# Performance work log

Hardware: AMD Instinct MI355X
Metric: run time of the kernel (lower is better)

## Reference

```python
import jax, jax.numpy as jnp
import numpy as np
from jax import lax

B, F, N = 1024, 512, 8  # batch, feature_dim, num_of_subAttention


def setup_inputs() -> dict:
    key = jax.random.key(0)
    ks = jax.random.split(key, 8)
    sc = 0.02
    return {
        "vx": jax.random.normal(ks[0], (B, F), dtype=jnp.float32),
        "ax": jax.random.normal(ks[1], (B, F), dtype=jnp.float32),
        # stacked per-unit MLP params (N units)
        "W1": jax.random.normal(ks[2], (N, F, 2 * F), dtype=jnp.float32) * sc,
        "b1": jnp.zeros((N, F), jnp.float32),
        "W2": jax.random.normal(ks[3], (N, F, F), dtype=jnp.float32) * sc,
        "b2": jnp.zeros((N, F), jnp.float32),
        # conv pipeline params (OIHW)
        "conv1_w": jax.random.normal(ks[4], (F, F, 3, 3), dtype=jnp.float32) * sc,
        "conv1_b": jnp.zeros((F,), jnp.float32),
        "conv2_w": jax.random.normal(ks[5], (F, F, 3, 3), dtype=jnp.float32) * sc,
        "conv2_b": jnp.zeros((F,), jnp.float32),
    }


def reference(vx, ax, W1, b1, W2, b2, conv1_w, conv1_b, conv2_w, conv2_b):
    # --- N AttentionUnits, vectorized over the unit axis n ---
    x = jnp.concatenate([vx, ax], axis=-1)                      # [B, 2F]
    # Dropout(0.5) is identity in eval mode.
    h = jax.nn.relu(jnp.einsum('bi,nfi->bnf', x, W1) + b1)      # [B, N, F]
    att = jax.nn.relu(jnp.einsum('bnf,ngf->bng', h, W2) + b2)   # [B, N, F]

    # vx broadcast over units, elementwise attention, then permute to [B, F, N]
    va = jnp.transpose(vx[:, None, :] * att, (0, 2, 1))         # [B, F, N]
    # rank-1 broadcast along trailing axis -> conv input [B, F, N, N]
    t = jnp.broadcast_to(va[..., None], (B, F, N, N))

    dn = ('NCHW', 'OIHW', 'NCHW')
    y = lax.conv_general_dilated(t, conv1_w, (1, 1), 'SAME', dimension_numbers=dn)
    y = y + conv1_b[None, :, None, None]
    k = N // 2
    y = lax.reduce_window(y, -jnp.inf, lax.max, (1, 1, k, k), (1, 1, k, k), 'VALID')  # [B,F,2,2]
    y = lax.conv_general_dilated(y, conv2_w, (1, 1), 'SAME', dimension_numbers=dn)
    y = y + conv2_b[None, :, None, None]
    y = jnp.mean(y, axis=(2, 3))                                # AdaptiveAvgPool2d((1,1)) -> [B, F]
    return jax.nn.relu(y)
```

## Files before the change

### kernel.cpp

```cpp
#include <hip/hip_runtime.h>
#include <hip/hip_bf16.h>


typedef __attribute__((ext_vector_type(8))) short short8;
typedef __attribute__((ext_vector_type(4))) float f32x4;

__device__ __forceinline__ void gload16(const void* g, void* l) {
    __builtin_amdgcn_global_load_lds(
        (const __attribute__((address_space(1))) void*)g,
        (__attribute__((address_space(3))) void*)l, 16, 0, 0);
}

template<int BM, int BN, bool RELU, bool BIAS, bool OUT_BF16>
__global__ __launch_bounds__(256) void gemm_mfma(
    const __hip_bfloat16* __restrict__ A, int lda, long sA,
    const __hip_bfloat16* __restrict__ B, int ldb, long sB,
    void* __restrict__ Cv, int ldc, long sC,
    const float* __restrict__ bias, long sBias,
    int K)
{
    constexpr int MI = BM / 32, NI = BN / 32;
    constexpr int GA = BM / 16, GB = BN / 16;
    constexpr int nA = (GA * 2) / 4, nB = (GB * 2) / 4;
    __shared__ __align__(16) char As[128 * BM];
    __shared__ __align__(16) char Bs[128 * BN];

    const int z = blockIdx.z;
    A += (long)z * sA;
    B += (long)z * sB;
    const int bm = blockIdx.y * BM;
    const int bn = blockIdx.x * BN;
    const int t = threadIdx.x, lane = t & 63, wid = t >> 6;
    const int q = lane >> 4, lr = lane & 15;
    const int wrow = (wid >> 1) * (BM / 2), wcol = (wid & 1) * (BN / 2);

    const int m_loc = lane >> 2;
    const int cst = ((lane & 3) - (m_loc >> 1)) & 3;
    const long abase = ((long)(bm + m_loc) * lda + cst * 8) * 2;
    const long bbase = ((long)(bn + m_loc) * ldb + cst * 8) * 2;
    const int ro = lr * 4;
    const int csel = (lr >> 1);

    f32x4 acc[MI][NI] = {};

    for (int k0 = 0; k0 < K; k0 += 64) {
        if (k0) __syncthreads();
        #pragma unroll
        for (int i = 0; i < nA; ++i) {
            int s = wid * nA + i, g = s % GA, h = s / GA;
            gload16((const char*)A + abase + ((long)g * 16 * lda + h * 32 + k0) * 2,
                    As + (h * (BM * 4) + g * 64) * 16);
        }
        #pragma unroll
        for (int i = 0; i < nB; ++i) {
            int s = wid * nB + i, g = s % GB, h = s / GB;
            gload16((const char*)B + bbase + ((long)g * 16 * ldb + h * 32 + k0) * 2,
                    Bs + (h * (BN * 4) + g * 64) * 16);
        }
        __syncthreads();

        #pragma unroll
        for (int ks = 0; ks < 2; ++ks) {
            short8 af[MI], bf[NI];
            #pragma unroll
            for (int mi = 0; mi < MI; ++mi) {
                int u = ks * (BM * 4) + ((wrow >> 4) + mi) * 64 + ro + ((q + csel) & 3);
                af[mi] = *(const short8*)(As + u * 16);
            }
            #pragma unroll
            for (int ni = 0; ni < NI; ++ni) {
                int u = ks * (BN * 4) + ((wcol >> 4) + ni) * 64 + ro + ((q + csel) & 3);
                bf[ni] = *(const short8*)(Bs + u * 16);
            }
            #pragma unroll
            for (int mi = 0; mi < MI; ++mi)
                #pragma unroll
                for (int ni = 0; ni < NI; ++ni)
                    acc[mi][ni] = __builtin_amdgcn_mfma_f32_16x16x32_bf16(
                        af[mi], bf[ni], acc[mi][ni], 0, 0, 0);
        }
    }

    #pragma unroll
    for (int mi = 0; mi < MI; ++mi) {
        #pragma unroll
        for (int ni = 0; ni < NI; ++ni) {
            int gn = bn + wcol + ni * 16 + lr;
            float bv = 0.f;
            if constexpr (BIAS) bv = bias[z * sBias + gn];
            #pragma unroll
            for (int r = 0; r < 4; ++r) {
                long gm = bm + wrow + mi * 16 + q * 4 + r;
                float v = acc[mi][ni][r] + bv;
                if constexpr (RELU) v = fmaxf(v, 0.f);
                if constexpr (OUT_BF16)
                    ((__hip_bfloat16*)Cv)[z * sC + gm * ldc + gn] = __float2bfloat16(v);
                else
                    ((float*)Cv)[z * sC + gm * ldc + gn] = v;
            }
        }
    }
}

__global__ __launch_bounds__(256) void conv_gemm_pool(
    const float* __restrict__ vx,
    const __hip_bfloat16* __restrict__ att,
    const __hip_bfloat16* __restrict__ B,
    float* __restrict__ PM)
{
    constexpr int BM = 128, BN = 128, MI = 4, NI = 4;
    constexpr int GB = 8, nB = 4;
    const int ldb = 1536;
    __shared__ __align__(16) char VAs[160 * 144];
    __shared__ __align__(16) char Bs[128 * BN];

    const int bm = blockIdx.x * BM;
    const int bn = blockIdx.y * BN;
    const int t = threadIdx.x, lane = t & 63, wid = t >> 6;
    const int q = lane >> 4, lr = lane & 15;
    const int wrow = (wid >> 1) * 64, wcol = (wid & 1) * 64;

    const int m_loc = lane >> 2;
    const int cstB = ((lane & 3) - (m_loc >> 1)) & 3;
    const long bbase = ((long)(bn + m_loc) * ldb + cstB * 8) * 2;
    const int ro = lr * 4;
    const int csel = (lr >> 1);

    {
        int b = t >> 4, side = (t >> 3) & 1, w8 = t & 7;
        int pr = b * 10 + side * 9;
        short8 z8 = {0, 0, 0, 0, 0, 0, 0, 0};
        *(short8*)(VAs + (pr * 9 + w8) * 16) = z8;
    }

    int abase_[MI];
    #pragma unroll
    for (int mi = 0; mi < MI; ++mi) {
        int m = wrow + mi * 16 + lr;
        abase_[mi] = (((m >> 3) * 10 + (m & 7)) * 9 + q) * 16;
    }

    f32x4 acc[MI][NI] = {};

    for (int kk = 0; kk < 24; ++kk) {
        const int ki = kk - (kk / 3) * 3;
        const int c0 = (kk / 3) << 6;
        const int k0B = ki * 512 + c0;
        if (kk) __syncthreads();
        #pragma unroll
        for (int i = 0; i < nB; ++i) {
            int s = wid * nB + i, g = s % GB, h = s / GB;
            gload16((const char*)B + bbase + ((long)g * 16 * ldb + k0B + h * 32) * 2,
                    Bs + (h * (BN * 4) + g * 64) * 16);
        }
        if (ki == 0) {
            #pragma unroll
            for (int u = 0; u < 4; ++u) {
                int li = t + u * 256;
                int r = li >> 3, w8 = li & 7;
                int gm = bm + r;
                int c = c0 + w8 * 8;
                short8 a8 = *(const short8*)(att + (long)gm * 512 + c);
                const float* vp = vx + ((gm >> 3) << 9) + c;
                float4 v0 = *(const float4*)vp;
                float4 v1 = *(const float4*)(vp + 4);
                float vf[8] = {v0.x, v0.y, v0.z, v0.w, v1.x, v1.y, v1.z, v1.w};
                short8 val;
                #pragma unroll
                for (int j = 0; j < 8; ++j) {
                    union { short s; __hip_bfloat16 h; } ua; ua.s = a8[j];
                    union { __hip_bfloat16 h; short s; } ub;
                    ub.h = __float2bfloat16(__bfloat162float(ua.h) * vf[j]);
                    val[j] = ub.s;
                }
                int pr = (r >> 3) * 10 + 1 + (r & 7);
                *(short8*)(VAs + (pr * 9 + w8) * 16) = val;
            }
        }
        __syncthreads();

        #pragma unroll
        for (int ks = 0; ks < 2; ++ks) {
            short8 af[MI], bf[NI];
            #pragma unroll
            for (int mi = 0; mi < MI; ++mi)
                af[mi] = *(const short8*)(VAs + abase_[mi] + ki * 144 + ks * 64);
            #pragma unroll
            for (int ni = 0; ni < NI; ++ni) {
                int u = ks * (BN * 4) + ((wcol >> 4) + ni) * 64 + ro + ((q + csel) & 3);
                bf[ni] = *(const short8*)(Bs + u * 16);
            }
            #pragma unroll
            for (int mi = 0; mi < MI; ++mi)
                #pragma unroll
                for (int ni = 0; ni < NI; ++ni)
                    acc[mi][ni] = __builtin_amdgcn_mfma_f32_16x16x32_bf16(
                        af[mi], bf[ni], acc[mi][ni], 0, 0, 0);
        }
    }

    #pragma unroll
    for (int mi = 0; mi < MI; ++mi) {
        int rowbase = bm + wrow + mi * 16;
        int batch = (rowbase >> 3) + (q >> 1);
        int pi = q & 1;
        #pragma unroll
        for (int ni = 0; ni < NI; ++ni) {
            int gn = bn + wcol + ni * 16 + lr;
            int v = gn >> 9, o = gn & 511;
            float m = fmaxf(fmaxf(acc[mi][ni][0], acc[mi][ni][1]),
                            fmaxf(acc[mi][ni][2], acc[mi][ni][3]));
            PM[((long)v * 1024 + batch) * 1024 + pi * 512 + o] = m;
        }
    }
}

__global__ __launch_bounds__(256) void prep_kernel(
    const float* __restrict__ vx, const float* __restrict__ ax,
    const float* __restrict__ W1, const float* __restrict__ W2,
    const float* __restrict__ c1w, const float* __restrict__ c2w,
    __hip_bfloat16* __restrict__ X,  __hip_bfloat16* __restrict__ W1b,
    __hip_bfloat16* __restrict__ W2b, __hip_bfloat16* __restrict__ WC,
    __hip_bfloat16* __restrict__ M2)
{
    int blk = blockIdx.x, t = threadIdx.x;
    if (blk < 2048) {
        int i = blk * 256 + t, b = i >> 9, c = i & 511;
        X[((long)b << 10) + c]       = __float2bfloat16(vx[i]);
        X[((long)b << 10) + 512 + c] = __float2bfloat16(ax[i]);
    } else if (blk < 8192) {
        int j = (blk - 2048) * 256 + t;
        const float* src = (j < 1048576) ? W1 : W2;
        __hip_bfloat16* dst = (j < 1048576) ? W1b : W2b;
        int k = (j < 1048576) ? j : j - 1048576;
        float4 v = ((const float4*)src)[k];
        union { __hip_bfloat16 h[4]; short4 s; } u;
        u.h[0] = __float2bfloat16(v.x); u.h[1] = __float2bfloat16(v.y);
        u.h[2] = __float2bfloat16(v.z); u.h[3] = __float2bfloat16(v.w);
        ((short4*)dst)[k] = u.s;
    } else if (blk < 17408) {
        int b2 = blk - 8192;
        int row = b2 / 6, col = (b2 % 6) * 256 + t;
        int v = row >> 9, o = row & 511;
        int ki = col >> 9, c = col & 511;
        const float* w = c1w + ((long)(o * 512 + c) * 3 + ki) * 3;
        float s = w[1];
        if (v != 0) s += w[0];
        if (v != 2) s += w[2];
        WC[(long)row * 1536 + col] = __float2bfloat16(s);
    } else {
        int b2 = blk - 17408;
        int o2 = b2 >> 3, col = (b2 & 7) * 256 + t;
        int c = col >> 2, pi = (col >> 1) & 1, pj = col & 1;
        const float* w = c2w + (long)(o2 * 512 + c) * 9;
        float s = w[pi * 3 + pj] + w[pi * 3 + pj + 1]
                + w[(pi + 1) * 3 + pj] + w[(pi + 1) * 3 + pj + 1];
        M2[(long)o2 * 2048 + col] = __float2bfloat16(0.25f * s);
    }
}

__global__ __launch_bounds__(256) void combine_kernel(
    const float* __restrict__ PM, const float* __restrict__ c1b,
    __hip_bfloat16* __restrict__ P)
{
    int idx = blockIdx.x * 256 + threadIdx.x;
    int b = idx >> 9, o = idx & 511;
    float bias = c1b[o];
    const long vs = 1024L * 1024;
    long base = (long)b * 1024 + o;
    float l0 = PM[base],            l1 = PM[base + 512];
    float m0 = PM[vs + base],       m1 = PM[vs + base + 512];
    float r0 = PM[2 * vs + base],   r1 = PM[2 * vs + base + 512];
    union { __hip_bfloat16 h[4]; short4 s; } u;
    u.h[0] = __float2bfloat16(fmaxf(l0, m0) + bias);
    u.h[1] = __float2bfloat16(fmaxf(m0, r0) + bias);
    u.h[2] = __float2bfloat16(fmaxf(l1, m1) + bias);
    u.h[3] = __float2bfloat16(fmaxf(m1, r1) + bias);
    ((short4*)(P + (long)b * 2048 + o * 4))[0] = u.s;
}

extern "C" void kernel_launch(void* const* d_in, const int* in_sizes, int n_in,
                              void* d_out, int out_size, void* d_ws, size_t ws_size,
                              hipStream_t stream)
{
    const float* vx  = (const float*)d_in[0];
    const float* ax  = (const float*)d_in[1];
    const float* W1  = (const float*)d_in[2];
    const float* b1  = (const float*)d_in[3];
    const float* W2  = (const float*)d_in[4];
    const float* b2  = (const float*)d_in[5];
    const float* c1w = (const float*)d_in[6];
    const float* c1b = (const float*)d_in[7];
    const float* c2w = (const float*)d_in[8];
    const float* c2b = (const float*)d_in[9];
    float* out = (float*)d_out;
    char* w = (char*)d_ws;

    const long MiB = 1 << 20;
    __hip_bfloat16* Xbf   = (__hip_bfloat16*)(w + 0 * MiB);
    __hip_bfloat16* W1bf  = (__hip_bfloat16*)(w + 2 * MiB);
    __hip_bfloat16* Hbf   = (__hip_bfloat16*)(w + 10 * MiB);
    __hip_bfloat16* W2bf  = (__hip_bfloat16*)(w + 18 * MiB);
    __hip_bfloat16* ATTbf = (__hip_bfloat16*)(w + 22 * MiB);
    __hip_bfloat16* WCbf  = (__hip_bfloat16*)(w + 30 * MiB);
    float*          PM    = (float*)         (w + 35 * MiB);
    __hip_bfloat16* Pbf   = (__hip_bfloat16*)(w + 47 * MiB);
    __hip_bfloat16* M2bf  = (__hip_bfloat16*)(w + 51 * MiB);

    prep_kernel<<<21504, 256, 0, stream>>>(vx, ax, W1, W2, c1w, c2w,
                                           Xbf, W1bf, W2bf, WCbf, M2bf);

    gemm_mfma<128, 128, true, true, true><<<dim3(32, 8, 1), 256, 0, stream>>>(
        Xbf, 1024, 0, W1bf, 1024, 0, Hbf, 4096, 0, b1, 0, 1024);

    gemm_mfma<128, 128, true, true, true><<<dim3(4, 8, 8), 256, 0, stream>>>(
        Hbf, 4096, 512, W2bf, 512, 262144, ATTbf, 4096, 512, b2, 512, 512);

    conv_gemm_pool<<<dim3(64, 12), 256, 0, stream>>>(vx, ATTbf, WCbf, PM);

    combine_kernel<<<2048, 256, 0, stream>>>(PM, c1b, Pbf);

    gemm_mfma<64, 64, true, true, false><<<dim3(8, 16, 1), 256, 0, stream>>>(
        Pbf, 2048, 0, M2bf, 2048, 0, out, 512, 0, c2b, 0, 2048);
}
```

Before: 208.9 us.

## Fuse pool-combine into output GEMM and store partial maxima in bf16

Removes the separate combine kernel and folds its max-over-neighbors plus bias step into the A-tile load of a new output GEMM kernel. The partial-max buffer PM is written in bf16 instead of fp32, halving its write and read traffic. The VA staging store in conv_gemm_pool also gets a rotated column assignment per row, presumably to cut LDS bank conflicts. This saves one launch and one round trip through memory, but PM is now recomputed redundantly in each N-tile of the output GEMM and rounded to bf16 one step earlier.

```diff
diff --git a/kernel.cpp b/kernel.cpp
--- a/kernel.cpp
+++ b/kernel.cpp
@@ -106,7 +106,7 @@
     const float* __restrict__ vx,
     const __hip_bfloat16* __restrict__ att,
     const __hip_bfloat16* __restrict__ B,
-    float* __restrict__ PM)
+    __hip_bfloat16* __restrict__ PM)
 {
     constexpr int BM = 128, BN = 128, MI = 4, NI = 4;
     constexpr int GB = 8, nB = 4;
@@ -157,7 +157,9 @@
             #pragma unroll
             for (int u = 0; u < 4; ++u) {
                 int li = t + u * 256;
-                int r = li >> 3, w8 = li & 7;
+                int r = li >> 3;
+                int pr = (r >> 3) * 10 + 1 + (r & 7);
+                int w8 = (t - pr) & 7;
                 int gm = bm + r;
                 int c = c0 + w8 * 8;
                 short8 a8 = *(const short8*)(att + (long)gm * 512 + c);
@@ -173,7 +175,6 @@
                     ub.h = __float2bfloat16(__bfloat162float(ua.h) * vf[j]);
                     val[j] = ub.s;
                 }
-                int pr = (r >> 3) * 10 + 1 + (r & 7);
                 *(short8*)(VAs + (pr * 9 + w8) * 16) = val;
             }
         }
@@ -210,7 +211,114 @@
             int v = gn >> 9, o = gn & 511;
             float m = fmaxf(fmaxf(acc[mi][ni][0], acc[mi][ni][1]),
                             fmaxf(acc[mi][ni][2], acc[mi][ni][3]));
-            PM[((long)v * 1024 + batch) * 1024 + pi * 512 + o] = m;
+            PM[(((long)v * 1024 + batch) * 2 + pi) * 512 + o] = __float2bfloat16(m);
+        }
+    }
+}
+
+__global__ __launch_bounds__(256) void out_gemm(
+    const __hip_bfloat16* __restrict__ PM,
+    const float* __restrict__ c1b,
+    const __hip_bfloat16* __restrict__ Bm,
+    const float* __restrict__ c2b,
+    float* __restrict__ out)
+{
+    constexpr int BM = 64, BN = 64, MI = 2, NI = 2;
+    constexpr int GB = 4, nB = 2;
+    const int ldb = 2048, K = 2048;
+    __shared__ __align__(16) char As[512 * 16];
+    __shared__ __align__(16) char Bs[512 * 16];
+
+    const int bm = blockIdx.y * BM, bn = blockIdx.x * BN;
+    const int t = threadIdx.x, lane = t & 63, wid = t >> 6;
+    const int q = lane >> 4, lr = lane & 15;
+    const int wrow = (wid >> 1) * 32, wcol = (wid & 1) * 32;
+    const int m_loc = lane >> 2;
+    const int cstB = ((lane & 3) - (m_loc >> 1)) & 3;
+    const long bbase = ((long)(bn + m_loc) * ldb + cstB * 8) * 2;
+    const int ro = lr * 4;
+    const int csel = (lr >> 1);
+
+    f32x4 acc[MI][NI] = {};
+
+    for (int k0 = 0; k0 < K; k0 += 64) {
+        if (k0) __syncthreads();
+        #pragma unroll
+        for (int i = 0; i < nB; ++i) {
+            int s = wid * nB + i, g = s % GB, h = s / GB;
+            gload16((const char*)Bm + bbase + ((long)g * 16 * ldb + h * 32 + k0) * 2,
+                    Bs + (h * (BN * 4) + g * 64) * 16);
+        }
+        #pragma unroll
+        for (int uu = 0; uu < 2; ++uu) {
+            int U = t + uu * 256;
+            int ks = U >> 8, m = (U >> 2) & 63, slot = U & 3;
+            int kc = (slot - (m >> 1)) & 3;
+            int kb = k0 + ks * 32 + kc * 8;
+            int o0 = kb >> 2;
+            int b = bm + m;
+            float pmv[3][2][2];
+            #pragma unroll
+            for (int v = 0; v < 3; ++v)
+                #pragma unroll
+                for (int pi = 0; pi < 2; ++pi) {
+                    const __hip_bfloat16* p =
+                        PM + (((long)v * 1024 + b) * 2 + pi) * 512 + o0;
+                    short2 s2 = *(const short2*)p;
+                    union { short s; __hip_bfloat16 h; } u0, u1;
+                    u0.s = s2.x; u1.s = s2.y;
+                    pmv[v][pi][0] = __bfloat162float(u0.h);
+                    pmv[v][pi][1] = __bfloat162float(u1.h);
+                }
+            float b0 = c1b[o0], b1 = c1b[o0 + 1];
+            short8 val;
+            #pragma unroll
+            for (int j = 0; j < 8; ++j) {
+                int os = j >> 2, pi = (j >> 1) & 1, pj = j & 1;
+                float a = (pj == 0) ? fmaxf(pmv[0][pi][os], pmv[1][pi][os])
+                                    : fmaxf(pmv[1][pi][os], pmv[2][pi][os]);
+                a += os ? b1 : b0;
+                union { __hip_bfloat16 h; short s; } ub;
+                ub.h = __float2bfloat16(a);
+                val[j] = ub.s;
+            }
+            *(short8*)(As + U * 16) = val;
+        }
+        __syncthreads();
+
+        #pragma unroll
+        for (int ks = 0; ks < 2; ++ks) {
+            short8 af[MI], bf[NI];
+            #pragma unroll
+            for (int mi = 0; mi < MI; ++mi) {
+                int u = ks * 256 + ((wrow >> 4) + mi) * 64 + ro + ((q + csel) & 3);
+                af[mi] = *(const short8*)(As + u * 16);
+            }
+            #pragma unroll
+            for (int ni = 0; ni < NI; ++ni) {
+                int u = ks * 256 + ((wcol >> 4) + ni) * 64 + ro + ((q + csel) & 3);
+                bf[ni] = *(const short8*)(Bs + u * 16);
+            }
+            #pragma unroll
+            for (int mi = 0; mi < MI; ++mi)
+                #pragma unroll
+                for (int ni = 0; ni < NI; ++ni)
+                    acc[mi][ni] = __builtin_amdgcn_mfma_f32_16x16x32_bf16(
+                        af[mi], bf[ni], acc[mi][ni], 0, 0, 0);
+        }
+    }
+
+    #pragma unroll
+    for (int mi = 0; mi < MI; ++mi) {
+        #pragma unroll
+        for (int ni = 0; ni < NI; ++ni) {
+            int gn = bn + wcol + ni * 16 + lr;
+            float bv = c2b[gn];
+            #pragma unroll
+            for (int r = 0; r < 4; ++r) {
+                long gm = bm + wrow + mi * 16 + q * 4 + r;
+                out[gm * 512 + gn] = fmaxf(acc[mi][ni][r] + bv, 0.f);
+            }
         }
     }
 }
@@ -259,26 +367,6 @@
     }
 }
 
-__global__ __launch_bounds__(256) void combine_kernel(
-    const float* __restrict__ PM, const float* __restrict__ c1b,
-    __hip_bfloat16* __restrict__ P)
-{
-    int idx = blockIdx.x * 256 + threadIdx.x;
-    int b = idx >> 9, o = idx & 511;
-    float bias = c1b[o];
-    const long vs = 1024L * 1024;
-    long base = (long)b * 1024 + o;
-    float l0 = PM[base],            l1 = PM[base + 512];
-    float m0 = PM[vs + base],       m1 = PM[vs + base + 512];
-    float r0 = PM[2 * vs + base],   r1 = PM[2 * vs + base + 512];
-    union { __hip_bfloat16 h[4]; short4 s; } u;
-    u.h[0] = __float2bfloat16(fmaxf(l0, m0) + bias);
-    u.h[1] = __float2bfloat16(fmaxf(m0, r0) + bias);
-    u.h[2] = __float2bfloat16(fmaxf(l1, m1) + bias);
-    u.h[3] = __float2bfloat16(fmaxf(m1, r1) + bias);
-    ((short4*)(P + (long)b * 2048 + o * 4))[0] = u.s;
-}
-
 extern "C" void kernel_launch(void* const* d_in, const int* in_sizes, int n_in,
                               void* d_out, int out_size, void* d_ws, size_t ws_size,
                               hipStream_t stream)
@@ -303,9 +391,8 @@
     __hip_bfloat16* W2bf  = (__hip_bfloat16*)(w + 18 * MiB);
     __hip_bfloat16* ATTbf = (__hip_bfloat16*)(w + 22 * MiB);
     __hip_bfloat16* WCbf  = (__hip_bfloat16*)(w + 30 * MiB);
-    float*          PM    = (float*)         (w + 35 * MiB);
-    __hip_bfloat16* Pbf   = (__hip_bfloat16*)(w + 47 * MiB);
-    __hip_bfloat16* M2bf  = (__hip_bfloat16*)(w + 51 * MiB);
+    __hip_bfloat16* PM    = (__hip_bfloat16*)(w + 35 * MiB);
+    __hip_bfloat16* M2bf  = (__hip_bfloat16*)(w + 41 * MiB);
 
     prep_kernel<<<21504, 256, 0, stream>>>(vx, ax, W1, W2, c1w, c2w,
                                            Xbf, W1bf, W2bf, WCbf, M2bf);
@@ -318,8 +405,5 @@
 
     conv_gemm_pool<<<dim3(64, 12), 256, 0, stream>>>(vx, ATTbf, WCbf, PM);
 
-    combine_kernel<<<2048, 256, 0, stream>>>(PM, c1b, Pbf);
-
-    gemm_mfma<64, 64, true, true, false><<<dim3(8, 16, 1), 256, 0, stream>>>(
-        Pbf, 2048, 0, M2bf, 2048, 0, out, 512, 0, c2b, 0, 2048);
-}
+    out_gemm<<<dim3(8, 16), 256, 0, stream>>>(PM, c1b, M2bf, c2b, out);
+}
```

Result: slower. 238.2 us (+14.0%).
